# Performance work log

Hardware: AMD Instinct MI355X
Metric: run time of the kernel (lower is better)

## Reference

```python
import jax, jax.numpy as jnp
import numpy as np
from jax import lax

K = 3
PAD = 1
STRIDE = 1
DIL = 1
BN_EPS = 1e-5


def bilinear_gather(x, py, px):
    """Zero-padded bilinear sampling. x:[B,C,Hin,Win]; py,px:[B,T,H,W] -> [B,C,T,H,W]."""
    B, C, Hin, Win = x.shape
    xf = x.reshape(B, C, Hin * Win)
    y0 = jnp.floor(py)
    x0 = jnp.floor(px)
    wy1 = py - y0
    wx1 = px - x0
    wy0 = 1.0 - wy1
    wx0 = 1.0 - wx1

    def corner(yc, xc, w):
        valid = (yc >= 0) & (yc <= Hin - 1) & (xc >= 0) & (xc <= Win - 1)
        yi = jnp.clip(yc, 0, Hin - 1).astype(jnp.int32)
        xi = jnp.clip(xc, 0, Win - 1).astype(jnp.int32)
        idx = (yi * Win + xi).reshape(B, -1)  # [B, T*H*W]
        vals = jax.vmap(lambda xb, ib: xb[:, ib])(xf, idx)  # [B, C, T*H*W]
        vals = vals.reshape(B, C, *py.shape[1:])
        return vals * (w * valid.astype(x.dtype))[:, None]

    return (corner(y0, x0, wy0 * wx0) + corner(y0, x0 + 1.0, wy0 * wx1)
            + corner(y0 + 1.0, x0, wy1 * wx0) + corner(y0 + 1.0, x0 + 1.0, wy1 * wx1))


def setup_inputs() -> dict:
    key = jax.random.key(0)
    ks = jax.random.split(key, 6)
    B, C, H, W, O = 8, 128, 80, 80, 128
    x = jax.random.normal(ks[0], (B, C, H, W), dtype=jnp.float32)
    # offset/mask conv (zero-init in the module; small random here so sampling is exercised)
    w_off = jax.random.normal(ks[1], (3 * K * K, C, K, K), dtype=jnp.float32) * 0.05
    b_off = jax.random.normal(ks[2], (3 * K * K,), dtype=jnp.float32) * 0.01
    # main DCN weight: uniform(-std, std), std = 1/sqrt(C*K*K)
    std = 1.0 / float(np.sqrt(C * K * K))
    w_dcn = jax.random.uniform(ks[3], (O, C, K, K), dtype=jnp.float32, minval=-std, maxval=std)
    b_dcn = jax.random.normal(ks[4], (O,), dtype=jnp.float32) * 0.01
    gamma = jnp.ones((O,), dtype=jnp.float32)
    beta = jnp.zeros((O,), dtype=jnp.float32)
    return {"x": x, "w_dcn": w_dcn, "b_dcn": b_dcn, "w_off": w_off, "b_off": b_off,
            "gamma": gamma, "beta": beta}


def reference(x, w_dcn, b_dcn, w_off, b_off, gamma, beta):
    B, C, H, W = x.shape
    O = w_dcn.shape[0]
    # offset/mask conv (k=3, s=1, p=1) -> [B, 27, H, W]
    om = lax.conv_general_dilated(x, w_off, (STRIDE, STRIDE), [(PAD, PAD), (PAD, PAD)],
                                  dimension_numbers=("NCHW", "OIHW", "NCHW"))
    om = om + b_off[None, :, None, None]
    o1, o2, m = jnp.split(om, 3, axis=1)  # each [B, 9, H, W]
    mask = jax.nn.sigmoid(m)
    # torch: offset = cat(o1, o2); torchvision reads channel 2t as dy_t, 2t+1 as dx_t
    off = jnp.concatenate([o1, o2], axis=1).reshape(B, K * K, 2, H, W)
    dy, dx = off[:, :, 0], off[:, :, 1]  # [B, 9, H, W]
    ky, kx = jnp.meshgrid(jnp.arange(K), jnp.arange(K), indexing="ij")
    ky = ky.reshape(-1)
    kx = kx.reshape(-1)  # [9]
    base_y = (jnp.arange(H)[None, :, None] * STRIDE - PAD + ky[:, None, None] * DIL).astype(x.dtype)  # [9,H,1]
    base_x = (jnp.arange(W)[None, None, :] * STRIDE - PAD + kx[:, None, None] * DIL).astype(x.dtype)  # [9,1,W]
    py = dy + base_y[None]  # [B, 9, H, W]
    px = dx + base_x[None]
    sampled = bilinear_gather(x, py, px)  # [B, C, 9, H, W]
    sampled = sampled * mask[:, None]  # modulated (dg=1 broadcasts over C)
    wk = w_dcn.reshape(O, C, K * K)
    out = jnp.einsum("bckhw,ock->bohw", sampled, wk) + b_dcn[None, :, None, None]
    # BatchNorm (training-mode batch stats, biased variance) + SiLU
    mu = out.mean(axis=(0, 2, 3), keepdims=True)
    var = out.var(axis=(0, 2, 3), keepdims=True)
    y = (out - mu) * lax.rsqrt(var + BN_EPS) * gamma[None, :, None, None] + beta[None, :, None, None]
    return y * jax.nn.sigmoid(y)
```

## Files before the change

kernel.cpp:

```cpp
#include <hip/hip_runtime.h>
#include <hip/hip_bf16.h>

constexpr int B = 8, C = 128, H = 80, W = 80, O = 128;
constexpr int HW = H * W;
constexpr int NPIX = B * HW;
constexpr int KC = C * 9;
constexpr int PX = 64;

typedef __attribute__((ext_vector_type(8))) short short8;
typedef __attribute__((ext_vector_type(4))) float f32x4;

__device__ inline ushort f2b(float f) {
  uint u = __float_as_uint(f);
  return (ushort)((u + 0x7FFFu + ((u >> 16) & 1u)) >> 16);
}
__device__ inline void unp(uint u, float& lo, float& hi) {
  lo = __uint_as_float(u << 16);
  hi = __uint_as_float(u & 0xFFFF0000u);
}
__device__ inline int swz16(int px, int byte) {
  return (px * 256 + (byte ^ ((px & 7) << 4))) >> 1;
}

__global__ __launch_bounds__(256) void k_xt(const float* __restrict__ x,
                                            ushort* __restrict__ xt) {
  const int t = threadIdx.x;
  const int g = t >> 4;
  const int hl = t & 15;
  const int p0 = blockIdx.x * 16;
  const int b = p0 / HW, hw = p0 - b * HW + hl;
  const float* xb = x + (size_t)b * C * HW + hw;
  uint u[4];
#pragma unroll
  for (int i = 0; i < 4; ++i) {
    float lo = xb[(size_t)(g * 8 + 2 * i) * HW];
    float hi = xb[(size_t)(g * 8 + 2 * i + 1) * HW];
    u[i] = (uint)f2b(lo) | ((uint)f2b(hi) << 16);
  }
  *(uint4*)(xt + ((size_t)b * HW + hw) * C + g * 8) = make_uint4(u[0], u[1], u[2], u[3]);
}

__global__ __launch_bounds__(256) void k_wt2(const float* __restrict__ w_dcn,
                                             const float* __restrict__ w_off,
                                             ushort* __restrict__ wt,
                                             ushort* __restrict__ wof) {
  int i = blockIdx.x * 256 + threadIdx.x;
  if (i < O * KC) {
    int c = i & 127, k = (i >> 7) % 9, o = i / KC;
    wt[i] = f2b(w_dcn[(size_t)o * KC + c * 9 + k]);
  }
  if (i < 32 * KC) {
    int c = i & 127, k = (i >> 7) % 9, o = i / KC;
    wof[i] = (o < 27) ? f2b(w_off[((size_t)o * C + c) * 9 + k]) : (ushort)0;
  }
}

__global__ __launch_bounds__(256, 4) void k_offc3(
    const ushort* __restrict__ xt, const ushort* __restrict__ wof,
    const float* __restrict__ b_off, float* __restrict__ om) {
  __shared__ __align__(16) ushort s_buf[2][PX * 128];
  const int t = threadIdx.x;
  const int bid = (blockIdx.x & 7) * 100 + (blockIdx.x >> 3);
  const int b = bid / 100, hw0 = (bid % 100) * PX;
  const int spx = t >> 2, sj = t & 3;
  const int hwp = hw0 + spx, hp = hwp / W, wp = hwp - hp * W;
  const ushort* xb = xt + (size_t)b * HW * C;
  uint4 ld[4];

  auto SLOAD = [&](int k) {
    int ky = k / 3, kx = k - ky * 3;
    int y = hp + ky - 1, xx = wp + kx - 1;
    bool ok = ((unsigned)y < (unsigned)H) && ((unsigned)xx < (unsigned)W);
    const ushort* r = xb + (size_t)(y * W + xx) * C + sj * 8;
#pragma unroll
    for (int e = 0; e < 4; ++e)
      ld[e] = ok ? *(const uint4*)(r + e * 32) : make_uint4(0u, 0u, 0u, 0u);
  };
  auto SWRITE = [&](ushort* buf) {
#pragma unroll
    for (int e = 0; e < 4; ++e)
      *(uint4*)(buf + swz16(spx, e * 64 + sj * 16)) = ld[e];
  };

  const int lane = t & 63, wv = t >> 6, rl = lane & 15, gh = lane >> 4;
  f32x4 acc[2] = {{0.f, 0.f, 0.f, 0.f}, {0.f, 0.f, 0.f, 0.f}};
  auto COMP = [&](const ushort* buf, int k) {
    const ushort* a0 = wof + (size_t)rl * KC + k * 128 + gh * 8;
#pragma unroll
    for (int kk = 0; kk < 128; kk += 32) {
      short8 av0 = *(const short8*)(a0 + kk);
      short8 av1 = *(const short8*)(a0 + 16 * KC + kk);
      short8 bv = *(const short8*)(buf + swz16(wv * 16 + rl, kk * 2 + gh * 16));
      acc[0] = __builtin_amdgcn_mfma_f32_16x16x32_bf16(av0, bv, acc[0], 0, 0, 0);
      acc[1] = __builtin_amdgcn_mfma_f32_16x16x32_bf16(av1, bv, acc[1], 0, 0, 0);
    }
  };

  SLOAD(0); SWRITE(s_buf[0]); __syncthreads();
  for (int k = 0; k < 9; ++k) {
    if (k < 8) SLOAD(k + 1);
    COMP(s_buf[k & 1], k);
    if (k < 8) { SWRITE(s_buf[(k + 1) & 1]); __syncthreads(); }
  }
  float* ob = om + (size_t)b * 27 * HW + hw0 + wv * 16 + rl;
#pragma unroll
  for (int m = 0; m < 2; ++m)
#pragma unroll
    for (int r = 0; r < 4; ++r) {
      int oc = m * 16 + gh * 4 + r;
      if (oc < 27) ob[(size_t)oc * HW] = acc[m][r] + b_off[oc];
    }
}

__global__ __launch_bounds__(256, 3) void k_dcn3(
    const ushort* __restrict__ xt, const float* __restrict__ om,
    const ushort* __restrict__ wt, float* __restrict__ outr) {
  __shared__ float s_w[PX][9][4];
  __shared__ int s_i[PX][9][4];
  __shared__ __align__(16) ushort s_buf[2][PX * 128];
  const int t = threadIdx.x;
  const int bid = (blockIdx.x & 7) * 100 + (blockIdx.x >> 3);
  const int b = bid / 100, hw0 = (bid % 100) * PX;

  for (int idx = t; idx < PX * 9; idx += 256) {
    int px = idx / 9, k = idx - (idx / 9) * 9;
    int hw = hw0 + px, h = hw / W, w = hw - (hw / W) * W;
    int ky = k / 3, kx = k - ky * 3;
    const float* omp = om + (size_t)b * 27 * HW + hw;
    float dy = omp[(size_t)(2 * k) * HW];
    float dx = omp[(size_t)(2 * k + 1) * HW];
    float mk = 1.0f / (1.0f + __expf(-omp[(size_t)(18 + k) * HW]));
    float py = dy + (float)(h - 1 + ky);
    float pxf = dx + (float)(w - 1 + kx);
    float y0f = floorf(py), x0f = floorf(pxf);
    float wy1 = py - y0f, wx1 = pxf - x0f;
    float wy0 = 1.0f - wy1, wx0 = 1.0f - wx1;
    int y0 = (int)y0f, x0 = (int)x0f;
    int y1 = y0 + 1, x1 = x0 + 1;
    bool vy0 = (y0 >= 0) && (y0 < H);
    bool vy1 = (y1 >= 0) && (y1 < H);
    bool vx0 = (x0 >= 0) && (x0 < W);
    bool vx1 = (x1 >= 0) && (x1 < W);
    int cy0 = min(max(y0, 0), H - 1), cy1 = min(max(y1, 0), H - 1);
    int cx0 = min(max(x0, 0), W - 1), cx1 = min(max(x1, 0), W - 1);
    s_w[px][k][0] = (vy0 && vx0) ? wy0 * wx0 * mk : 0.0f;
    s_w[px][k][1] = (vy0 && vx1) ? wy0 * wx1 * mk : 0.0f;
    s_w[px][k][2] = (vy1 && vx0) ? wy1 * wx0 * mk : 0.0f;
    s_w[px][k][3] = (vy1 && vx1) ? wy1 * wx1 * mk : 0.0f;
    s_i[px][k][0] = cy0 * W + cx0;
    s_i[px][k][1] = cy0 * W + cx1;
    s_i[px][k][2] = cy1 * W + cx0;
    s_i[px][k][3] = cy1 * W + cx1;
  }
  __syncthreads();

  const int spx = t >> 2, sj = t & 3;
  const ushort* xb = xt + (size_t)b * HW * C + sj * 8;
  uint4 ld[4][4];
  float cw0, cw1, cw2, cw3;

  auto SLOAD = [&](int k) {
    int4 ii = *(const int4*)&s_i[spx][k][0];
    float4 wwv = *(const float4*)&s_w[spx][k][0];
    cw0 = wwv.x; cw1 = wwv.y; cw2 = wwv.z; cw3 = wwv.w;
    const ushort* r0 = xb + (size_t)ii.x * C;
    const ushort* r1 = xb + (size_t)ii.y * C;
    const ushort* r2 = xb + (size_t)ii.z * C;
    const ushort* r3 = xb + (size_t)ii.w * C;
#pragma unroll
    for (int e = 0; e < 4; ++e) {
      ld[0][e] = *(const uint4*)(r0 + e * 32);
      ld[1][e] = *(const uint4*)(r1 + e * 32);
      ld[2][e] = *(const uint4*)(r2 + e * 32);
      ld[3][e] = *(const uint4*)(r3 + e * 32);
    }
  };
  auto SWRITE = [&](ushort* buf) {
#pragma unroll
    for (int e = 0; e < 4; ++e) {
      uint q0[4] = {ld[0][e].x, ld[0][e].y, ld[0][e].z, ld[0][e].w};
      uint q1[4] = {ld[1][e].x, ld[1][e].y, ld[1][e].z, ld[1][e].w};
      uint q2[4] = {ld[2][e].x, ld[2][e].y, ld[2][e].z, ld[2][e].w};
      uint q3[4] = {ld[3][e].x, ld[3][e].y, ld[3][e].z, ld[3][e].w};
      uint r[4];
#pragma unroll
      for (int d = 0; d < 4; ++d) {
        float a0, a1, b0, b1, c0, c1, d0, d1;
        unp(q0[d], a0, a1);
        unp(q1[d], b0, b1);
        unp(q2[d], c0, c1);
        unp(q3[d], d0, d1);
        float vlo = fmaf(cw3, d0, fmaf(cw2, c0, fmaf(cw1, b0, cw0 * a0)));
        float vhi = fmaf(cw3, d1, fmaf(cw2, c1, fmaf(cw1, b1, cw0 * a1)));
        r[d] = (uint)f2b(vlo) | ((uint)f2b(vhi) << 16);
      }
      *(uint4*)(buf + swz16(spx, e * 64 + sj * 16)) = make_uint4(r[0], r[1], r[2], r[3]);
    }
  };

  const int lane = t & 63, wv = t >> 6, rl = lane & 15, gh = lane >> 4;
  f32x4 acc[2][4];
#pragma unroll
  for (int m = 0; m < 2; ++m)
#pragma unroll
    for (int nt = 0; nt < 4; ++nt) acc[m][nt] = {0.f, 0.f, 0.f, 0.f};

  auto COMP = [&](const ushort* buf, int k) {
    const ushort* a0 = wt + (size_t)(wv * 32 + rl) * KC + k * 128 + gh * 8;
    __builtin_amdgcn_s_setprio(1);
#pragma unroll
    for (int kk = 0; kk < 128; kk += 32) {
      short8 av0 = *(const short8*)(a0 + kk);
      short8 av1 = *(const short8*)(a0 + 16 * KC + kk);
#pragma unroll
      for (int nt = 0; nt < 4; ++nt) {
        short8 bv = *(const short8*)(buf + swz16(nt * 16 + rl, kk * 2 + gh * 16));
        acc[0][nt] = __builtin_amdgcn_mfma_f32_16x16x32_bf16(av0, bv, acc[0][nt], 0, 0, 0);
        acc[1][nt] = __builtin_amdgcn_mfma_f32_16x16x32_bf16(av1, bv, acc[1][nt], 0, 0, 0);
      }
    }
    __builtin_amdgcn_s_setprio(0);
  };

  SLOAD(0); SWRITE(s_buf[0]); __syncthreads();
  for (int k = 0; k < 9; ++k) {
    if (k < 8) SLOAD(k + 1);
    COMP(s_buf[k & 1], k);
    if (k < 8) { SWRITE(s_buf[(k + 1) & 1]); __syncthreads(); }
  }
  float* outb = outr + (size_t)b * O * HW + hw0 + rl;
#pragma unroll
  for (int m = 0; m < 2; ++m)
#pragma unroll
    for (int nt = 0; nt < 4; ++nt)
#pragma unroll
      for (int r = 0; r < 4; ++r)
        outb[(size_t)(wv * 32 + m * 16 + gh * 4 + r) * HW + nt * 16] = acc[m][nt][r];
}

__global__ __launch_bounds__(256) void k_bnstats2(const float* __restrict__ outr,
                                                  float* __restrict__ part) {
  const int o = blockIdx.x >> 2, pb = blockIdx.x & 3;
  float s = 0.f, s2 = 0.f;
  for (int i = threadIdx.x; i < 2 * HW / 4; i += 256) {
    int bb = i / (HW / 4);
    float4 v = ((const float4*)(outr + ((size_t)(2 * pb + bb) * O + o) * HW))[i - bb * (HW / 4)];
    s += v.x + v.y + v.z + v.w;
    s2 = fmaf(v.x, v.x, s2);
    s2 = fmaf(v.y, v.y, s2);
    s2 = fmaf(v.z, v.z, s2);
    s2 = fmaf(v.w, v.w, s2);
  }
#pragma unroll
  for (int off = 32; off > 0; off >>= 1) {
    s += __shfl_down(s, off);
    s2 += __shfl_down(s2, off);
  }
  __shared__ float rs[4], rs2[4];
  int wid = threadIdx.x >> 6, lane = threadIdx.x & 63;
  if (lane == 0) { rs[wid] = s; rs2[wid] = s2; }
  __syncthreads();
  if (threadIdx.x == 0) {
    float S = rs[0] + rs[1] + rs[2] + rs[3];
    float S2 = rs2[0] + rs2[1] + rs2[2] + rs2[3];
    part[(o * 4 + pb) * 2] = S;
    part[(o * 4 + pb) * 2 + 1] = S2;
  }
}

__global__ __launch_bounds__(256) void k_bnapply2(
    float* __restrict__ outr, const float* __restrict__ part,
    const float* __restrict__ gamma, const float* __restrict__ beta) {
  const int n4 = B * O * HW / 4;
  for (int i = blockIdx.x * blockDim.x + threadIdx.x; i < n4;
       i += gridDim.x * blockDim.x) {
    int o = (i / (HW / 4)) % O;
    float S = 0.f, S2 = 0.f;
#pragma unroll
    for (int pb = 0; pb < 4; ++pb) {
      S += part[(o * 4 + pb) * 2];
      S2 += part[(o * 4 + pb) * 2 + 1];
    }
    const float inv = 1.0f / (float)(B * HW);
    float mu = S * inv;
    float rstd = rsqrtf(fmaf(S2, inv, -mu * mu) + 1e-5f);
    float a = rstd * gamma[o];
    float bb = fmaf(-mu, a, beta[o]);
    float4 v = ((const float4*)outr)[i];
    float y0 = fmaf(v.x, a, bb);
    float y1 = fmaf(v.y, a, bb);
    float y2 = fmaf(v.z, a, bb);
    float y3 = fmaf(v.w, a, bb);
    v.x = y0 / (1.0f + __expf(-y0));
    v.y = y1 / (1.0f + __expf(-y1));
    v.z = y2 / (1.0f + __expf(-y2));
    v.w = y3 / (1.0f + __expf(-y3));
    ((float4*)outr)[i] = v;
  }
}

extern "C" void kernel_launch(void* const* d_in, const int* in_sizes, int n_in,
                              void* d_out, int out_size, void* d_ws, size_t ws_size,
                              hipStream_t stream) {
  const float* x = (const float*)d_in[0];
  const float* w_dcn = (const float*)d_in[1];
  const float* w_off = (const float*)d_in[3];
  const float* b_off = (const float*)d_in[4];
  const float* gamma = (const float*)d_in[5];
  const float* beta = (const float*)d_in[6];
  float* out = (float*)d_out;
  float* om = (float*)d_ws;
  ushort* xt = (ushort*)(om + (size_t)B * 27 * HW);
  ushort* wt = xt + (size_t)B * HW * C;
  ushort* wof = wt + (size_t)O * KC;
  float* part = (float*)(wof + (size_t)32 * KC);

  k_xt<<<NPIX / 16, 256, 0, stream>>>(x, xt);
  k_wt2<<<(O * KC + 255) / 256, 256, 0, stream>>>(w_dcn, w_off, wt, wof);
  k_offc3<<<NPIX / PX, 256, 0, stream>>>(xt, wof, b_off, om);
  k_dcn3<<<NPIX / PX, 256, 0, stream>>>(xt, om, wt, out);
  k_bnstats2<<<O * 4, 256, 0, stream>>>(out, part);
  k_bnapply2<<<2048, 256, 0, stream>>>(out, part, gamma, beta);
}
```

Baseline: 211.9 us.

## Fuse BN stats into DCN kernel, halve pixel tile, drop LDS in offset conv

The DCN kernel now accumulates per-channel sum and sum-of-squares with shuffle reductions and atomics, which removes the separate stats kernel and its full re-read of the output. The pixel tile is halved to 32 with per-wave 2x2 MFMA tiles and higher occupancy, and gathers use inline asm wide loads with explicit waitcnt. The offset conv reads operands straight from global memory through a zero-row pointer instead of staging in LDS. Atomics add nondeterministic summation order, and smaller tiles reload weights more often.

```diff
diff --git a/kernel.cpp b/kernel.cpp
--- a/kernel.cpp
+++ b/kernel.cpp
@@ -5,7 +5,7 @@
 constexpr int HW = H * W;
 constexpr int NPIX = B * HW;
 constexpr int KC = C * 9;
-constexpr int PX = 64;
+constexpr int PX = 32;
 
 typedef __attribute__((ext_vector_type(8))) short short8;
 typedef __attribute__((ext_vector_type(4))) float f32x4;
@@ -17,6 +17,10 @@
 __device__ inline void unp(uint u, float& lo, float& hi) {
   lo = __uint_as_float(u << 16);
   hi = __uint_as_float(u & 0xFFFF0000u);
+}
+__device__ inline uint pk2(float lo, float hi) {
+  __hip_bfloat162 h = __float22bfloat162_rn(make_float2(lo, hi));
+  return *reinterpret_cast<uint*>(&h);
 }
 __device__ inline int swz16(int px, int byte) {
   return (px * 256 + (byte ^ ((px & 7) << 4))) >> 1;
@@ -43,7 +47,9 @@
 __global__ __launch_bounds__(256) void k_wt2(const float* __restrict__ w_dcn,
                                              const float* __restrict__ w_off,
                                              ushort* __restrict__ wt,
-                                             ushort* __restrict__ wof) {
+                                             ushort* __restrict__ wof,
+                                             float* __restrict__ part,
+                                             ushort* __restrict__ zrow) {
   int i = blockIdx.x * 256 + threadIdx.x;
   if (i < O * KC) {
     int c = i & 127, k = (i >> 7) % 9, o = i / KC;
@@ -53,74 +59,55 @@
     int c = i & 127, k = (i >> 7) % 9, o = i / KC;
     wof[i] = (o < 27) ? f2b(w_off[((size_t)o * C + c) * 9 + k]) : (ushort)0;
   }
-}
-
-__global__ __launch_bounds__(256, 4) void k_offc3(
+  if (i < 256) part[i] = 0.0f;
+  if (i < 128) zrow[i] = 0;
+}
+
+__global__ __launch_bounds__(256, 6) void k_offc4(
     const ushort* __restrict__ xt, const ushort* __restrict__ wof,
-    const float* __restrict__ b_off, float* __restrict__ om) {
-  __shared__ __align__(16) ushort s_buf[2][PX * 128];
+    const ushort* __restrict__ zrow, const float* __restrict__ b_off,
+    float* __restrict__ om) {
   const int t = threadIdx.x;
-  const int bid = (blockIdx.x & 7) * 100 + (blockIdx.x >> 3);
-  const int b = bid / 100, hw0 = (bid % 100) * PX;
-  const int spx = t >> 2, sj = t & 3;
-  const int hwp = hw0 + spx, hp = hwp / W, wp = hwp - hp * W;
+  const int bid = (blockIdx.x & 7) * 200 + (blockIdx.x >> 3);
+  const int b = bid / 200, hw0 = (bid - b * 200) * PX;
+  const int lane = t & 63, wv = t >> 6, rl = lane & 15, gh = lane >> 4;
+  const int mi = wv & 1, nt = wv >> 1;
+  const int px = hw0 + nt * 16 + rl;
+  const int hp = px / W, wp = px - hp * W;
   const ushort* xb = xt + (size_t)b * HW * C;
-  uint4 ld[4];
-
-  auto SLOAD = [&](int k) {
+  f32x4 acc = {0.f, 0.f, 0.f, 0.f};
+#pragma unroll
+  for (int k = 0; k < 9; ++k) {
     int ky = k / 3, kx = k - ky * 3;
     int y = hp + ky - 1, xx = wp + kx - 1;
     bool ok = ((unsigned)y < (unsigned)H) && ((unsigned)xx < (unsigned)W);
-    const ushort* r = xb + (size_t)(y * W + xx) * C + sj * 8;
-#pragma unroll
-    for (int e = 0; e < 4; ++e)
-      ld[e] = ok ? *(const uint4*)(r + e * 32) : make_uint4(0u, 0u, 0u, 0u);
-  };
-  auto SWRITE = [&](ushort* buf) {
-#pragma unroll
-    for (int e = 0; e < 4; ++e)
-      *(uint4*)(buf + swz16(spx, e * 64 + sj * 16)) = ld[e];
-  };
-
-  const int lane = t & 63, wv = t >> 6, rl = lane & 15, gh = lane >> 4;
-  f32x4 acc[2] = {{0.f, 0.f, 0.f, 0.f}, {0.f, 0.f, 0.f, 0.f}};
-  auto COMP = [&](const ushort* buf, int k) {
-    const ushort* a0 = wof + (size_t)rl * KC + k * 128 + gh * 8;
-#pragma unroll
-    for (int kk = 0; kk < 128; kk += 32) {
-      short8 av0 = *(const short8*)(a0 + kk);
-      short8 av1 = *(const short8*)(a0 + 16 * KC + kk);
-      short8 bv = *(const short8*)(buf + swz16(wv * 16 + rl, kk * 2 + gh * 16));
-      acc[0] = __builtin_amdgcn_mfma_f32_16x16x32_bf16(av0, bv, acc[0], 0, 0, 0);
-      acc[1] = __builtin_amdgcn_mfma_f32_16x16x32_bf16(av1, bv, acc[1], 0, 0, 0);
-    }
-  };
-
-  SLOAD(0); SWRITE(s_buf[0]); __syncthreads();
-  for (int k = 0; k < 9; ++k) {
-    if (k < 8) SLOAD(k + 1);
-    COMP(s_buf[k & 1], k);
-    if (k < 8) { SWRITE(s_buf[(k + 1) & 1]); __syncthreads(); }
-  }
-  float* ob = om + (size_t)b * 27 * HW + hw0 + wv * 16 + rl;
-#pragma unroll
-  for (int m = 0; m < 2; ++m)
-#pragma unroll
-    for (int r = 0; r < 4; ++r) {
-      int oc = m * 16 + gh * 4 + r;
-      if (oc < 27) ob[(size_t)oc * HW] = acc[m][r] + b_off[oc];
-    }
-}
-
-__global__ __launch_bounds__(256, 3) void k_dcn3(
+    const ushort* rowp = ok ? (xb + (size_t)(y * W + xx) * C) : zrow;
+    const ushort* aP = wof + (size_t)(mi * 16 + rl) * KC + k * 128 + gh * 8;
+#pragma unroll
+    for (int kk = 0; kk < 4; ++kk) {
+      short8 av = *(const short8*)(aP + kk * 32);
+      short8 bv = *(const short8*)(rowp + kk * 32 + gh * 8);
+      acc = __builtin_amdgcn_mfma_f32_16x16x32_bf16(av, bv, acc, 0, 0, 0);
+    }
+  }
+  float* ob = om + (size_t)b * 27 * HW + hw0 + nt * 16 + rl;
+#pragma unroll
+  for (int r = 0; r < 4; ++r) {
+    int oc = mi * 16 + gh * 4 + r;
+    if (oc < 27) ob[(size_t)oc * HW] = acc[r] + b_off[oc];
+  }
+}
+
+__global__ __launch_bounds__(256, 4) void k_dcn3(
     const ushort* __restrict__ xt, const float* __restrict__ om,
-    const ushort* __restrict__ wt, float* __restrict__ outr) {
+    const ushort* __restrict__ wt, float* __restrict__ outr,
+    float* __restrict__ part) {
   __shared__ float s_w[PX][9][4];
   __shared__ int s_i[PX][9][4];
   __shared__ __align__(16) ushort s_buf[2][PX * 128];
   const int t = threadIdx.x;
-  const int bid = (blockIdx.x & 7) * 100 + (blockIdx.x >> 3);
-  const int b = bid / 100, hw0 = (bid % 100) * PX;
+  const int bid = (blockIdx.x & 7) * 200 + (blockIdx.x >> 3);
+  const int b = bid / 200, hw0 = (bid - b * 200) * PX;
 
   for (int idx = t; idx < PX * 9; idx += 256) {
     int px = idx / 9, k = idx - (idx / 9) * 9;
@@ -154,117 +141,113 @@
   }
   __syncthreads();
 
-  const int spx = t >> 2, sj = t & 3;
-  const ushort* xb = xt + (size_t)b * HW * C + sj * 8;
-  uint4 ld[4][4];
+  const int sp = t >> 3, sq = t & 7;
+  const ushort* xbq = xt + (size_t)b * HW * C + sq * 16;
+  uint4 lA0, lA1, lB0, lB1, lC0, lC1, lD0, lD1;
   float cw0, cw1, cw2, cw3;
 
   auto SLOAD = [&](int k) {
-    int4 ii = *(const int4*)&s_i[spx][k][0];
-    float4 wwv = *(const float4*)&s_w[spx][k][0];
-    cw0 = wwv.x; cw1 = wwv.y; cw2 = wwv.z; cw3 = wwv.w;
-    const ushort* r0 = xb + (size_t)ii.x * C;
-    const ushort* r1 = xb + (size_t)ii.y * C;
-    const ushort* r2 = xb + (size_t)ii.z * C;
-    const ushort* r3 = xb + (size_t)ii.w * C;
-#pragma unroll
-    for (int e = 0; e < 4; ++e) {
-      ld[0][e] = *(const uint4*)(r0 + e * 32);
-      ld[1][e] = *(const uint4*)(r1 + e * 32);
-      ld[2][e] = *(const uint4*)(r2 + e * 32);
-      ld[3][e] = *(const uint4*)(r3 + e * 32);
-    }
+    int4 ii = *(const int4*)&s_i[sp][k][0];
+    float4 wf = *(const float4*)&s_w[sp][k][0];
+    cw0 = wf.x; cw1 = wf.y; cw2 = wf.z; cw3 = wf.w;
+    const ushort* r0 = xbq + (size_t)ii.x * C;
+    const ushort* r1 = xbq + (size_t)ii.y * C;
+    const ushort* r2 = xbq + (size_t)ii.z * C;
+    const ushort* r3 = xbq + (size_t)ii.w * C;
+    asm volatile("global_load_dwordx4 %0, %2, off\n\t"
+                 "global_load_dwordx4 %1, %2, off offset:16"
+                 : "=&v"(lA0), "=&v"(lA1) : "v"(r0));
+    asm volatile("global_load_dwordx4 %0, %2, off\n\t"
+                 "global_load_dwordx4 %1, %2, off offset:16"
+                 : "=&v"(lB0), "=&v"(lB1) : "v"(r1));
+    asm volatile("global_load_dwordx4 %0, %2, off\n\t"
+                 "global_load_dwordx4 %1, %2, off offset:16"
+                 : "=&v"(lC0), "=&v"(lC1) : "v"(r2));
+    asm volatile("global_load_dwordx4 %0, %2, off\n\t"
+                 "global_load_dwordx4 %1, %2, off offset:16"
+                 : "=&v"(lD0), "=&v"(lD1) : "v"(r3));
   };
+
   auto SWRITE = [&](ushort* buf) {
-#pragma unroll
-    for (int e = 0; e < 4; ++e) {
-      uint q0[4] = {ld[0][e].x, ld[0][e].y, ld[0][e].z, ld[0][e].w};
-      uint q1[4] = {ld[1][e].x, ld[1][e].y, ld[1][e].z, ld[1][e].w};
-      uint q2[4] = {ld[2][e].x, ld[2][e].y, ld[2][e].z, ld[2][e].w};
-      uint q3[4] = {ld[3][e].x, ld[3][e].y, ld[3][e].z, ld[3][e].w};
-      uint r[4];
-#pragma unroll
-      for (int d = 0; d < 4; ++d) {
-        float a0, a1, b0, b1, c0, c1, d0, d1;
-        unp(q0[d], a0, a1);
-        unp(q1[d], b0, b1);
-        unp(q2[d], c0, c1);
-        unp(q3[d], d0, d1);
-        float vlo = fmaf(cw3, d0, fmaf(cw2, c0, fmaf(cw1, b0, cw0 * a0)));
-        float vhi = fmaf(cw3, d1, fmaf(cw2, c1, fmaf(cw1, b1, cw0 * a1)));
-        r[d] = (uint)f2b(vlo) | ((uint)f2b(vhi) << 16);
-      }
-      *(uint4*)(buf + swz16(spx, e * 64 + sj * 16)) = make_uint4(r[0], r[1], r[2], r[3]);
-    }
+    uint qa[8] = {lA0.x, lA0.y, lA0.z, lA0.w, lA1.x, lA1.y, lA1.z, lA1.w};
+    uint qb[8] = {lB0.x, lB0.y, lB0.z, lB0.w, lB1.x, lB1.y, lB1.z, lB1.w};
+    uint qc[8] = {lC0.x, lC0.y, lC0.z, lC0.w, lC1.x, lC1.y, lC1.z, lC1.w};
+    uint qd[8] = {lD0.x, lD0.y, lD0.z, lD0.w, lD1.x, lD1.y, lD1.z, lD1.w};
+    uint r[8];
+#pragma unroll
+    for (int d = 0; d < 8; ++d) {
+      float a0, a1, b0, b1, c0, c1, d0, d1;
+      unp(qa[d], a0, a1);
+      unp(qb[d], b0, b1);
+      unp(qc[d], c0, c1);
+      unp(qd[d], d0, d1);
+      float vlo = fmaf(cw3, d0, fmaf(cw2, c0, fmaf(cw1, b0, cw0 * a0)));
+      float vhi = fmaf(cw3, d1, fmaf(cw2, c1, fmaf(cw1, b1, cw0 * a1)));
+      r[d] = pk2(vlo, vhi);
+    }
+    *(uint4*)(buf + swz16(sp, sq * 32)) = make_uint4(r[0], r[1], r[2], r[3]);
+    *(uint4*)(buf + swz16(sp, sq * 32 + 16)) = make_uint4(r[4], r[5], r[6], r[7]);
   };
 
   const int lane = t & 63, wv = t >> 6, rl = lane & 15, gh = lane >> 4;
-  f32x4 acc[2][4];
-#pragma unroll
-  for (int m = 0; m < 2; ++m)
-#pragma unroll
-    for (int nt = 0; nt < 4; ++nt) acc[m][nt] = {0.f, 0.f, 0.f, 0.f};
+  f32x4 acc00 = {0.f, 0.f, 0.f, 0.f}, acc01 = acc00, acc10 = acc00, acc11 = acc00;
 
   auto COMP = [&](const ushort* buf, int k) {
-    const ushort* a0 = wt + (size_t)(wv * 32 + rl) * KC + k * 128 + gh * 8;
+    const ushort* aP = wt + (size_t)(wv * 32 + rl) * KC + k * 128 + gh * 8;
     __builtin_amdgcn_s_setprio(1);
 #pragma unroll
-    for (int kk = 0; kk < 128; kk += 32) {
-      short8 av0 = *(const short8*)(a0 + kk);
-      short8 av1 = *(const short8*)(a0 + 16 * KC + kk);
-#pragma unroll
-      for (int nt = 0; nt < 4; ++nt) {
-        short8 bv = *(const short8*)(buf + swz16(nt * 16 + rl, kk * 2 + gh * 16));
-        acc[0][nt] = __builtin_amdgcn_mfma_f32_16x16x32_bf16(av0, bv, acc[0][nt], 0, 0, 0);
-        acc[1][nt] = __builtin_amdgcn_mfma_f32_16x16x32_bf16(av1, bv, acc[1][nt], 0, 0, 0);
-      }
+    for (int kk = 0; kk < 4; ++kk) {
+      short8 av0 = *(const short8*)(aP + kk * 32);
+      short8 av1 = *(const short8*)(aP + (size_t)16 * KC + kk * 32);
+      short8 bv0 = *(const short8*)(buf + swz16(rl, kk * 64 + gh * 16));
+      short8 bv1 = *(const short8*)(buf + swz16(16 + rl, kk * 64 + gh * 16));
+      acc00 = __builtin_amdgcn_mfma_f32_16x16x32_bf16(av0, bv0, acc00, 0, 0, 0);
+      acc01 = __builtin_amdgcn_mfma_f32_16x16x32_bf16(av0, bv1, acc01, 0, 0, 0);
+      acc10 = __builtin_amdgcn_mfma_f32_16x16x32_bf16(av1, bv0, acc10, 0, 0, 0);
+      acc11 = __builtin_amdgcn_mfma_f32_16x16x32_bf16(av1, bv1, acc11, 0, 0, 0);
     }
     __builtin_amdgcn_s_setprio(0);
   };
 
-  SLOAD(0); SWRITE(s_buf[0]); __syncthreads();
+  SLOAD(0);
+  asm volatile("s_waitcnt vmcnt(0)" ::: "memory");
+  __builtin_amdgcn_sched_barrier(0);
+  SWRITE(s_buf[0]);
+  __syncthreads();
   for (int k = 0; k < 9; ++k) {
     if (k < 8) SLOAD(k + 1);
     COMP(s_buf[k & 1], k);
-    if (k < 8) { SWRITE(s_buf[(k + 1) & 1]); __syncthreads(); }
-  }
+    __builtin_amdgcn_sched_barrier(0);
+    if (k < 8) {
+      asm volatile("s_waitcnt vmcnt(0)" ::: "memory");
+      __builtin_amdgcn_sched_barrier(0);
+      SWRITE(s_buf[(k + 1) & 1]);
+      __syncthreads();
+    }
+  }
+
   float* outb = outr + (size_t)b * O * HW + hw0 + rl;
 #pragma unroll
-  for (int m = 0; m < 2; ++m)
-#pragma unroll
-    for (int nt = 0; nt < 4; ++nt)
-#pragma unroll
-      for (int r = 0; r < 4; ++r)
-        outb[(size_t)(wv * 32 + m * 16 + gh * 4 + r) * HW + nt * 16] = acc[m][nt][r];
-}
-
-__global__ __launch_bounds__(256) void k_bnstats2(const float* __restrict__ outr,
-                                                  float* __restrict__ part) {
-  const int o = blockIdx.x >> 2, pb = blockIdx.x & 3;
-  float s = 0.f, s2 = 0.f;
-  for (int i = threadIdx.x; i < 2 * HW / 4; i += 256) {
-    int bb = i / (HW / 4);
-    float4 v = ((const float4*)(outr + ((size_t)(2 * pb + bb) * O + o) * HW))[i - bb * (HW / 4)];
-    s += v.x + v.y + v.z + v.w;
-    s2 = fmaf(v.x, v.x, s2);
-    s2 = fmaf(v.y, v.y, s2);
-    s2 = fmaf(v.z, v.z, s2);
-    s2 = fmaf(v.w, v.w, s2);
-  }
-#pragma unroll
-  for (int off = 32; off > 0; off >>= 1) {
-    s += __shfl_down(s, off);
-    s2 += __shfl_down(s2, off);
-  }
-  __shared__ float rs[4], rs2[4];
-  int wid = threadIdx.x >> 6, lane = threadIdx.x & 63;
-  if (lane == 0) { rs[wid] = s; rs2[wid] = s2; }
-  __syncthreads();
-  if (threadIdx.x == 0) {
-    float S = rs[0] + rs[1] + rs[2] + rs[3];
-    float S2 = rs2[0] + rs2[1] + rs2[2] + rs2[3];
-    part[(o * 4 + pb) * 2] = S;
-    part[(o * 4 + pb) * 2 + 1] = S2;
+  for (int mi = 0; mi < 2; ++mi) {
+    f32x4 a0 = mi ? acc10 : acc00;
+    f32x4 a1 = mi ? acc11 : acc01;
+#pragma unroll
+    for (int r = 0; r < 4; ++r) {
+      int o = wv * 32 + mi * 16 + gh * 4 + r;
+      outb[(size_t)o * HW] = a0[r];
+      outb[(size_t)o * HW + 16] = a1[r];
+      float s = a0[r] + a1[r];
+      float s2 = fmaf(a0[r], a0[r], a1[r] * a1[r]);
+#pragma unroll
+      for (int m = 1; m < 16; m <<= 1) {
+        s += __shfl_xor(s, m);
+        s2 += __shfl_xor(s2, m);
+      }
+      if (rl == 0) {
+        atomicAdd(&part[2 * o], s);
+        atomicAdd(&part[2 * o + 1], s2);
+      }
+    }
   }
 }
 
@@ -275,12 +258,7 @@
   for (int i = blockIdx.x * blockDim.x + threadIdx.x; i < n4;
        i += gridDim.x * blockDim.x) {
     int o = (i / (HW / 4)) % O;
-    float S = 0.f, S2 = 0.f;
-#pragma unroll
-    for (int pb = 0; pb < 4; ++pb) {
-      S += part[(o * 4 + pb) * 2];
-      S2 += part[(o * 4 + pb) * 2 + 1];
-    }
+    float S = part[2 * o], S2 = part[2 * o + 1];
     const float inv = 1.0f / (float)(B * HW);
     float mu = S * inv;
     float rstd = rsqrtf(fmaf(S2, inv, -mu * mu) + 1e-5f);
@@ -314,11 +292,11 @@
   ushort* wt = xt + (size_t)B * HW * C;
   ushort* wof = wt + (size_t)O * KC;
   float* part = (float*)(wof + (size_t)32 * KC);
+  ushort* zrow = (ushort*)(part + 256);
 
   k_xt<<<NPIX / 16, 256, 0, stream>>>(x, xt);
-  k_wt2<<<(O * KC + 255) / 256, 256, 0, stream>>>(w_dcn, w_off, wt, wof);
-  k_offc3<<<NPIX / PX, 256, 0, stream>>>(xt, wof, b_off, om);
-  k_dcn3<<<NPIX / PX, 256, 0, stream>>>(xt, om, wt, out);
-  k_bnstats2<<<O * 4, 256, 0, stream>>>(out, part);
+  k_wt2<<<(O * KC + 255) / 256, 256, 0, stream>>>(w_dcn, w_off, wt, wof, part, zrow);
+  k_offc4<<<NPIX / PX, 256, 0, stream>>>(xt, wof, zrow, b_off, om);
+  k_dcn3<<<NPIX / PX, 256, 0, stream>>>(xt, om, wt, out, part);
   k_bnapply2<<<2048, 256, 0, stream>>>(out, part, gamma, beta);
 }
```

Result: slower. 514.1 us (+142.7%).
